# Kernel optimization log

Measured on AMD Instinct MI355X. Metric: run time of the kernel, lower is better.

The kernel has to match this reference:

```python
import jax, jax.numpy as jnp
import numpy as np

E = 262144   # number of edges
B = 8192     # buckets per grouping
D = 32       # uniform bucket degree (B*D == E)
DIM = 128    # in_feats
OUT = 128    # out_feats


def setup_inputs() -> dict:
    key = jax.random.key(0)
    ks = jax.random.split(key, 12)
    src_feat = jax.random.normal(ks[0], (E, DIM), jnp.float32)
    dst_feat = jax.random.normal(ks[1], (E, DIM), jnp.float32)
    timestamp = jax.random.uniform(ks[2], (E,), jnp.float32) * 100.0
    # grouping permutations: flat edge order -> buckets of uniform degree
    src_perm = jax.random.permutation(ks[3], E).astype(jnp.int32)
    dst_perm = jax.random.permutation(ks[4], E).astype(jnp.int32)
    # causal deg_indices: index of most recent valid temporal neighbor, <= position
    pos = jnp.arange(D, dtype=jnp.int32)[None, :]
    src_deg_indices = jnp.minimum(jax.random.randint(ks[5], (B, D), 0, D, jnp.int32), pos)
    dst_deg_indices = jnp.minimum(jax.random.randint(ks[6], (B, D), 0, D, jnp.int32), pos)
    # TimeEncodingLayer('cosine') params
    basis_freq = 0.1 * jnp.linspace(0.0, 9.0, DIM, dtype=jnp.float32)
    phase = jnp.zeros((DIM,), jnp.float32)
    W_time = jax.random.normal(ks[7], (DIM, 2 * DIM), jnp.float32) * 0.05
    b_time = jnp.zeros((DIM,), jnp.float32)
    # fc_self / fc_neigh
    W_self = jax.random.normal(ks[8], (OUT, DIM), jnp.float32) * 0.05
    b_self = jnp.zeros((OUT,), jnp.float32)
    W_neigh = jax.random.normal(ks[9], (OUT, DIM), jnp.float32) * 0.05
    b_neigh = jnp.zeros((OUT,), jnp.float32)
    return dict(src_feat=src_feat, dst_feat=dst_feat, timestamp=timestamp,
                basis_freq=basis_freq, phase=phase, W_time=W_time, b_time=b_time,
                W_self=W_self, b_self=b_self, W_neigh=W_neigh, b_neigh=b_neigh,
                src_perm=src_perm, dst_perm=dst_perm,
                src_deg_indices=src_deg_indices, dst_deg_indices=dst_deg_indices)


def _encode_time(u, t, basis_freq, phase, W_time, b_time):
    # cosine time encoding: cos(t * freq + phase), concat with u, linear, relu
    tt = jnp.cos(t[:, None] * basis_freq[None, :] + phase[None, :])  # [E, DIM]
    x = jnp.concatenate([u, tt], axis=-1) @ W_time.T + b_time
    return jax.nn.relu(x)


def _mean_conv(h_self_e, h_neigh_e, perm, idx, W_self, b_self, W_neigh, b_neigh):
    # gather flat edge features into [B, D, DIM] buckets
    hs = h_self_e[perm].reshape(B, D, DIM)
    hn = h_neigh_e[perm].reshape(B, D, DIM)
    # mean aggregator: cumsum / (deg_indices+1), then gather at deg_indices
    mean_cof = (idx.astype(hn.dtype) + 1.0)[:, :, None]          # [B, D, 1]
    h_feat = jnp.cumsum(hn, axis=1) / mean_cof                    # [B, D, DIM]
    mask_feat = jnp.take_along_axis(h_feat, idx[:, :, None], axis=1)  # [B, D, DIM]
    rst = hs @ W_self.T + b_self + mask_feat @ W_neigh.T + b_neigh    # [B, D, OUT]
    # scatter back to flat edge order
    return jnp.zeros((E, OUT), rst.dtype).at[perm].set(rst.reshape(E, OUT))


def reference(src_feat, dst_feat, timestamp, basis_freq, phase, W_time, b_time,
              W_self, b_self, W_neigh, b_neigh,
              src_perm, dst_perm, src_deg_indices, dst_deg_indices):
    enc_src = _encode_time(src_feat, timestamp, basis_freq, phase, W_time, b_time)
    enc_dst = _encode_time(dst_feat, timestamp, basis_freq, phase, W_time, b_time)
    # groupby='src': self = src embedding, neighbors = dst embeddings
    src_out = _mean_conv(enc_src, enc_dst, src_perm, src_deg_indices,
                         W_self, b_self, W_neigh, b_neigh)
    # groupby='dst': self = dst embedding, neighbors = src embeddings
    dst_out = _mean_conv(enc_dst, enc_src, dst_perm, dst_deg_indices,
                         W_self, b_self, W_neigh, b_neigh)
    return src_out, dst_out
```

## Files before the change

### kernel.cpp

```cpp
#include <hip/hip_runtime.h>
#include <hip/hip_bf16.h>
#include <math.h>

#define E_EDGES 262144
#define NBUCKET 8192
#define DEG     32
#define FDIM    128

typedef float f32x4 __attribute__((ext_vector_type(4)));
typedef short s16x8 __attribute__((ext_vector_type(8)));
typedef short s16x4 __attribute__((ext_vector_type(4)));

typedef const __attribute__((address_space(1))) unsigned g_u32;
typedef __attribute__((address_space(3))) unsigned l_u32;

__device__ __forceinline__ short f2bf(float f) {
    __hip_bfloat16 h = __float2bfloat16(f);
    return *reinterpret_cast<short*>(&h);
}
__device__ __forceinline__ float bf2f(short s) {
    union { unsigned u; float f; } v; v.u = ((unsigned)(unsigned short)s) << 16;
    return v.f;
}

__device__ __forceinline__ s16x8 read_wfrag(const short* w_lds, int n, int k0) {
    int byte = ((n << 8) + (k0 << 1)) ^ ((n & 7) << 4);
    return *reinterpret_cast<const s16x8*>(reinterpret_cast<const char*>(w_lds) + byte);
}

__device__ __forceinline__ void stage_w(short* w_lds, const float* __restrict__ Wg,
                                        int stride, int tid) {
    #pragma unroll
    for (int it = 0; it < 16; ++it) {
        int i  = it * 256 + tid;
        int n  = i >> 5;
        int k4 = (i & 31) << 2;
        const float4 v = *reinterpret_cast<const float4*>(Wg + (size_t)n * stride + k4);
        s16x4 h; h[0]=f2bf(v.x); h[1]=f2bf(v.y); h[2]=f2bf(v.z); h[3]=f2bf(v.w);
        int byte = ((n << 8) + (k4 << 1)) ^ ((n & 7) << 4);
        *reinterpret_cast<s16x4*>(reinterpret_cast<char*>(w_lds) + byte) = h;
    }
}

__device__ __forceinline__ void dma_w32k(const short* __restrict__ gsw, short* lds, int tid) {
    const int lane = tid & 63, wid = tid >> 6;
    const char* g = reinterpret_cast<const char*>(gsw);
    char* l = reinterpret_cast<char*>(lds);
    #pragma unroll
    for (int i = 0; i < 8; ++i) {
        const int off = i * 4096 + wid * 1024;
        __builtin_amdgcn_global_load_lds((g_u32*)(g + off + lane * 16),
                                         (l_u32*)(l + off), 16, 0, 0);
    }
}

__global__ void prep_kernel(const float* __restrict__ W_time,
                            const float* __restrict__ W_self,
                            const float* __restrict__ W_neigh,
                            const float* __restrict__ b_self,
                            const float* __restrict__ b_neigh,
                            short* __restrict__ Wswz,
                            float* __restrict__ bsum)
{
    const int t = blockIdx.x * 256 + threadIdx.x;
    if (t < 8192) {
        const int region = t >> 11;
        const int chunk  = t & 2047;
        const int n = chunk >> 4;
        const int c = chunk & 15;

        const float* src;
        if      (region == 0) src = W_time  + n * 256 + c * 8;
        else if (region == 1) src = W_time  + n * 256 + 128 + c * 8;
        else if (region == 2) src = W_self  + n * 128 + c * 8;
        else                  src = W_neigh + n * 128 + c * 8;

        const float4 lo = *reinterpret_cast<const float4*>(src);
        const float4 hi = *reinterpret_cast<const float4*>(src + 4);
        s16x8 h;
        h[0]=f2bf(lo.x); h[1]=f2bf(lo.y); h[2]=f2bf(lo.z); h[3]=f2bf(lo.w);
        h[4]=f2bf(hi.x); h[5]=f2bf(hi.y); h[6]=f2bf(hi.z); h[7]=f2bf(hi.w);

        const int byte = (region << 15) + ((((n << 8) + (c << 4)) ^ ((n & 7) << 4)));
        *reinterpret_cast<s16x8*>(reinterpret_cast<char*>(Wswz) + byte) = h;
    } else if (t < 8192 + 128) {
        const int c = t - 8192;
        bsum[c] = b_self[c] + b_neigh[c];
    }
}

__global__ __launch_bounds__(512, 4)
void encode_kernel(const float* __restrict__ src_feat,
                   const float* __restrict__ dst_feat,
                   const float* __restrict__ ts,
                   const float* __restrict__ freq,
                   const float* __restrict__ ph,
                   const short* __restrict__ Wswz,
                   const float* __restrict__ b_time,
                   short* __restrict__ enc_src,
                   short* __restrict__ enc_dst)
{
    __shared__ short w_lds[2][128 * 128];

    const int tid  = threadIdx.x;
    const int lane = tid & 63;
    const int wid  = tid >> 6;
    const int lrow = lane & 15;
    const int q    = lane >> 4;
    const int klo  = q << 3;
    const int r0   = blockIdx.x * 128 + wid * 16;

    float4 sf[8], df[8];
    #pragma unroll
    for (int kb = 0; kb < 4; ++kb) {
        const float* ps = src_feat + (size_t)(r0 + lrow) * FDIM + kb * 32 + klo;
        const float* pd = dst_feat + (size_t)(r0 + lrow) * FDIM + kb * 32 + klo;
        sf[kb*2]   = *reinterpret_cast<const float4*>(ps);
        sf[kb*2+1] = *reinterpret_cast<const float4*>(ps + 4);
        df[kb*2]   = *reinterpret_cast<const float4*>(pd);
        df[kb*2+1] = *reinterpret_cast<const float4*>(pd + 4);
    }

    {
        const char* g = reinterpret_cast<const char*>(Wswz);
        char* l = reinterpret_cast<char*>(&w_lds[0][0]);
        #pragma unroll
        for (int i = 0; i < 8; ++i) {
            const int off = i * 8192 + wid * 1024;
            __builtin_amdgcn_global_load_lds((g_u32*)(g + off + lane * 16),
                                             (l_u32*)(l + off), 16, 0, 0);
        }
    }

    const float t_row = ts[r0 + lrow];
    s16x8 tf[4];
    #pragma unroll
    for (int kb = 0; kb < 4; ++kb) {
        s16x8 t;
        #pragma unroll
        for (int j = 0; j < 8; ++j) {
            const int k = kb * 32 + klo + j;
            t[j] = f2bf(__cosf(fmaf(t_row, freq[k], ph[k])));
        }
        tf[kb] = t;
    }

    s16x8 as_[4], ad_[4];
    #pragma unroll
    for (int kb = 0; kb < 4; ++kb) {
        s16x8 a, b;
        #pragma unroll
        for (int j = 0; j < 4; ++j) {
            a[j]   = f2bf(sf[kb*2][j]);   a[4+j] = f2bf(sf[kb*2+1][j]);
            b[j]   = f2bf(df[kb*2][j]);   b[4+j] = f2bf(df[kb*2+1][j]);
        }
        as_[kb] = a; ad_[kb] = b;
    }
    __syncthreads();

    #pragma unroll
    for (int nt = 0; nt < 8; ++nt) {
        const int n = nt * 16 + lrow;
        f32x4 a = {0.f, 0.f, 0.f, 0.f};
        #pragma unroll
        for (int kb = 0; kb < 4; ++kb)
            a = __builtin_amdgcn_mfma_f32_16x16x32_bf16(
                    read_wfrag(w_lds[1], n, kb * 32 + klo), tf[kb], a, 0, 0, 0);
        f32x4 b = a;
        #pragma unroll
        for (int kb = 0; kb < 4; ++kb) {
            const s16x8 wf = read_wfrag(w_lds[0], n, kb * 32 + klo);
            a = __builtin_amdgcn_mfma_f32_16x16x32_bf16(wf, as_[kb], a, 0, 0, 0);
            b = __builtin_amdgcn_mfma_f32_16x16x32_bf16(wf, ad_[kb], b, 0, 0, 0);
        }
        const int ch = nt * 16 + q * 4;
        const float4 bias4 = *reinterpret_cast<const float4*>(b_time + ch);
        s16x4 ss, sd;
        #pragma unroll
        for (int r = 0; r < 4; ++r) {
            float es = a[r] + bias4[r]; es = es > 0.f ? es : 0.f;
            float ed = b[r] + bias4[r]; ed = ed > 0.f ? ed : 0.f;
            ss[r] = f2bf(es); sd[r] = f2bf(ed);
        }
        *reinterpret_cast<s16x4*>(enc_src + (size_t)(r0 + lrow) * FDIM + ch) = ss;
        *reinterpret_cast<s16x4*>(enc_dst + (size_t)(r0 + lrow) * FDIM + ch) = sd;
    }
}

__global__ __launch_bounds__(256, 2)
void encode_fallback(const float* __restrict__ src_feat,
                     const float* __restrict__ dst_feat,
                     const float* __restrict__ ts,
                     const float* __restrict__ freq,
                     const float* __restrict__ ph,
                     const float* __restrict__ W_time,
                     const float* __restrict__ b_time,
                     short* __restrict__ enc_src,
                     short* __restrict__ enc_dst)
{
    __shared__ short w_lds[128 * 128];
    const int tid  = threadIdx.x;
    const int lane = tid & 63;
    const int wid  = tid >> 6;
    const int r0   = blockIdx.x * 64 + wid * 16;
    const int lrow = lane & 15;
    const int klo  = (lane >> 4) << 3;

    stage_w(w_lds, W_time + 128, 256, tid);
    const float t_row = ts[r0 + lrow];
    s16x8 tf[4];
    #pragma unroll
    for (int kb = 0; kb < 4; ++kb) {
        const int k = kb * 32 + klo;
        s16x8 t;
        #pragma unroll
        for (int j = 0; j < 8; ++j)
            t[j] = f2bf(__cosf(fmaf(t_row, freq[k + j], ph[k + j])));
        tf[kb] = t;
    }
    __syncthreads();
    f32x4 S[8];
    #pragma unroll
    for (int nt = 0; nt < 8; ++nt) {
        f32x4 a = {0.f, 0.f, 0.f, 0.f};
        #pragma unroll
        for (int kb = 0; kb < 4; ++kb)
            a = __builtin_amdgcn_mfma_f32_16x16x32_bf16(
                    tf[kb], read_wfrag(w_lds, nt * 16 + lrow, kb * 32 + klo), a, 0, 0, 0);
        S[nt] = a;
    }
    __syncthreads();
    stage_w(w_lds, W_time, 256, tid);
    __syncthreads();
    #pragma unroll
    for (int s = 0; s < 2; ++s) {
        const float* feat = s ? dst_feat : src_feat;
        short*       enc  = s ? enc_dst  : enc_src;
        s16x8 af[4];
        #pragma unroll
        for (int kb = 0; kb < 4; ++kb) {
            const float* p = feat + (size_t)(r0 + lrow) * FDIM + kb * 32 + klo;
            const float4 lo = *reinterpret_cast<const float4*>(p);
            const float4 hi = *reinterpret_cast<const float4*>(p + 4);
            s16x8 a;
            a[0]=f2bf(lo.x); a[1]=f2bf(lo.y); a[2]=f2bf(lo.z); a[3]=f2bf(lo.w);
            a[4]=f2bf(hi.x); a[5]=f2bf(hi.y); a[6]=f2bf(hi.z); a[7]=f2bf(hi.w);
            af[kb] = a;
        }
        #pragma unroll
        for (int nt = 0; nt < 8; ++nt) {
            f32x4 acc = S[nt];
            #pragma unroll
            for (int kb = 0; kb < 4; ++kb)
                acc = __builtin_amdgcn_mfma_f32_16x16x32_bf16(
                        af[kb], read_wfrag(w_lds, nt * 16 + lrow, kb * 32 + klo), acc, 0, 0, 0);
            const int col  = nt * 16 + lrow;
            const float bias = b_time[col];
            const int rbase = r0 + ((lane >> 4) << 2);
            #pragma unroll
            for (int r = 0; r < 4; ++r) {
                float e = acc[r] + bias;
                e = e > 0.f ? e : 0.f;
                enc[(size_t)(rbase + r) * FDIM + col] = f2bf(e);
            }
        }
    }
}

template<int DMA>
__global__ __launch_bounds__(256, 3)
void conv_kernel(const short* __restrict__ enc_src,
                 const short* __restrict__ enc_dst,
                 const short* __restrict__ Wswz_self,
                 const short* __restrict__ Wswz_neigh,
                 const float* __restrict__ W_self,
                 const float* __restrict__ W_neigh,
                 const float* __restrict__ bsum,
                 const float* __restrict__ b_self,
                 const float* __restrict__ b_neigh,
                 const int* __restrict__ src_perm,
                 const int* __restrict__ dst_perm,
                 const int* __restrict__ src_idx,
                 const int* __restrict__ dst_idx,
                 float* __restrict__ out)
{
    __shared__ short w_lds[128 * 128];
    __shared__ short hf[2][DEG * 128];
    __shared__ int   perm_s[2][DEG];
    __shared__ int   idx_s[2][DEG];

    const int tid = threadIdx.x;
    const int g   = blockIdx.y;
    const int b0  = blockIdx.x * 2;

    const short* enc_self  = g ? enc_dst : enc_src;
    const short* enc_neigh = g ? enc_src : enc_dst;
    const int*   perm      = g ? dst_perm : src_perm;
    const int*   degi      = g ? dst_idx  : src_idx;
    float*       outg      = out + (size_t)g * E_EDGES * FDIM;

    if (DMA) dma_w32k(Wswz_self, w_lds, tid);

    if (tid < 64) {
        const int lb = tid >> 5, d = tid & 31;
        perm_s[lb][d] = perm[(b0 + lb) * DEG + d];
        idx_s[lb][d]  = degi[(b0 + lb) * DEG + d];
    }
    if (!DMA) stage_w(w_lds, W_self, 128, tid);
    __syncthreads();

    const int lane = tid & 63;
    const int wid  = tid >> 6;
    const int lb   = wid >> 1;
    const int mt   = wid & 1;
    const int lrow = lane & 15;
    const int q    = lane >> 4;
    const int klo  = q << 3;
    const int row  = mt * 16 + lrow;

    s16x8 hsf[4];
    {
        const int e = perm_s[lb][row];
        const short* p = enc_self + (size_t)e * FDIM;
        #pragma unroll
        for (int kb = 0; kb < 4; ++kb)
            hsf[kb] = *reinterpret_cast<const s16x8*>(p + kb * 32 + klo);
    }

    unsigned cum[DEG];
    if (wid < 2) {
        #pragma unroll
        for (int d = 0; d < DEG; ++d) {
            const int e = perm_s[wid][d];
            cum[d] = *reinterpret_cast<const unsigned*>(
                         enc_neigh + (size_t)e * FDIM + 2 * lane);
        }
    }

    f32x4 acc[8];
    #pragma unroll
    for (int nt = 0; nt < 8; ++nt) {
        f32x4 a = {0.f, 0.f, 0.f, 0.f};
        #pragma unroll
        for (int kb = 0; kb < 4; ++kb)
            a = __builtin_amdgcn_mfma_f32_16x16x32_bf16(
                    read_wfrag(w_lds, nt * 16 + lrow, kb * 32 + klo), hsf[kb], a, 0, 0, 0);
        acc[nt] = a;
    }

    if (wid < 2) {
        float run0 = 0.f, run1 = 0.f;
        #pragma unroll
        for (int d = 0; d < DEG; ++d) {
            run0 += bf2f((short)(cum[d] & 0xFFFFu));
            run1 += bf2f((short)(cum[d] >> 16));
            const float inv = __builtin_amdgcn_rcpf((float)(idx_s[wid][d] + 1));
            const unsigned pk = (unsigned)(unsigned short)f2bf(run0 * inv)
                              | ((unsigned)(unsigned short)f2bf(run1 * inv) << 16);
            const int byte = ((d << 8) + (lane << 2)) ^ ((d & 7) << 4);
            *reinterpret_cast<unsigned*>(reinterpret_cast<char*>(hf[wid]) + byte) = pk;
        }
    }

    __syncthreads();
    if (DMA) dma_w32k(Wswz_neigh, w_lds, tid);
    else     stage_w(w_lds, W_neigh, 128, tid);
    __syncthreads();

    s16x8 mff[4];
    {
        const int j = idx_s[lb][row];
        #pragma unroll
        for (int kb = 0; kb < 4; ++kb) {
            const int byte = ((j << 8) + ((kb * 32 + klo) << 1)) ^ ((j & 7) << 4);
            mff[kb] = *reinterpret_cast<const s16x8*>(
                          reinterpret_cast<const char*>(hf[lb]) + byte);
        }
    }
    #pragma unroll
    for (int nt = 0; nt < 8; ++nt) {
        f32x4 a = acc[nt];
        #pragma unroll
        for (int kb = 0; kb < 4; ++kb)
            a = __builtin_amdgcn_mfma_f32_16x16x32_bf16(
                    read_wfrag(w_lds, nt * 16 + lrow, kb * 32 + klo), mff[kb], a, 0, 0, 0);
        acc[nt] = a;
    }

    {
        const int e = perm_s[lb][row];
        float* po = outg + (size_t)e * FDIM;
        #pragma unroll
        for (int nt = 0; nt < 8; ++nt) {
            const int ch = nt * 16 + q * 4;
            float4 bs4;
            if (DMA) bs4 = *reinterpret_cast<const float4*>(bsum + ch);
            else {
                const float4 s4 = *reinterpret_cast<const float4*>(b_self + ch);
                const float4 n4 = *reinterpret_cast<const float4*>(b_neigh + ch);
                bs4 = make_float4(s4.x+n4.x, s4.y+n4.y, s4.z+n4.z, s4.w+n4.w);
            }
            f32x4 v;
            v[0] = acc[nt][0] + bs4.x; v[1] = acc[nt][1] + bs4.y;
            v[2] = acc[nt][2] + bs4.z; v[3] = acc[nt][3] + bs4.w;
            *reinterpret_cast<f32x4*>(po + ch) = v;
        }
    }
}

extern "C" void kernel_launch(void* const* d_in, const int* in_sizes, int n_in,
                              void* d_out, int out_size, void* d_ws, size_t ws_size,
                              hipStream_t stream) {
    (void)in_sizes; (void)n_in; (void)out_size;

    const float* src_feat = (const float*)d_in[0];
    const float* dst_feat = (const float*)d_in[1];
    const float* ts       = (const float*)d_in[2];
    const float* freq     = (const float*)d_in[3];
    const float* ph       = (const float*)d_in[4];
    const float* W_time   = (const float*)d_in[5];
    const float* b_time   = (const float*)d_in[6];
    const float* W_self   = (const float*)d_in[7];
    const float* b_self   = (const float*)d_in[8];
    const float* W_neigh  = (const float*)d_in[9];
    const float* b_neigh  = (const float*)d_in[10];
    const int*   src_perm = (const int*)d_in[11];
    const int*   dst_perm = (const int*)d_in[12];
    const int*   src_idx  = (const int*)d_in[13];
    const int*   dst_idx  = (const int*)d_in[14];

    short* enc_src = (short*)d_ws;
    short* enc_dst = enc_src + (size_t)E_EDGES * FDIM;
    short* Wswz    = enc_dst + (size_t)E_EDGES * FDIM;
    float* bsum    = (float*)(Wswz + 4 * 16384);
    const size_t need = (size_t)E_EDGES * FDIM * 2 * 2 + 4 * 32768 + 512;

    if (ws_size >= need) {
        prep_kernel<<<dim3(33), dim3(256), 0, stream>>>(
            W_time, W_self, W_neigh, b_self, b_neigh, Wswz, bsum);
        encode_kernel<<<dim3(E_EDGES / 128), dim3(512), 0, stream>>>(
            src_feat, dst_feat, ts, freq, ph, Wswz, b_time, enc_src, enc_dst);
        conv_kernel<1><<<dim3(NBUCKET / 2, 2), dim3(256), 0, stream>>>(
            enc_src, enc_dst, Wswz + 2 * 16384, Wswz + 3 * 16384, W_self, W_neigh,
            bsum, b_self, b_neigh, src_perm, dst_perm, src_idx, dst_idx, (float*)d_out);
    } else {
        encode_fallback<<<dim3(E_EDGES / 64), dim3(256), 0, stream>>>(
            src_feat, dst_feat, ts, freq, ph, W_time, b_time, enc_src, enc_dst);
        conv_kernel<0><<<dim3(NBUCKET / 2, 2), dim3(256), 0, stream>>>(
            enc_src, enc_dst, (const short*)nullptr, (const short*)nullptr,
            W_self, W_neigh, (const float*)nullptr, b_self, b_neigh,
            src_perm, dst_perm, src_idx, dst_idx, (float*)d_out);
    }
}
```

Measured before the change: 254.2 us.

## Project neighbor features before prefix-mean via triangular-mask MFMA

The serial per-bucket cumulative sum is removed. It used to run in two waves followed by a gather of prefix rows. Each wave now projects its own neighbor rows through W_neigh first, stores the projected rows as bf16 in LDS, and applies the causal prefix-mean as a single MFMA per output tile. That MFMA uses a lower-triangular mask vector scaled by 1/(idx[idx[row]]+1). This spreads the neighbor loads and scan work across all waves instead of serialising it in two. In exchange it adds an extra barrier and an LDS round trip of the projected values, and rounding to bf16 after projection slightly changes numerics.

Measured after the change: 257.4 us. No clear change (+1.3%).

```diff
diff --git a/kernel.cpp b/kernel.cpp
--- a/kernel.cpp
+++ b/kernel.cpp
@@ -285,7 +285,7 @@
                  float* __restrict__ out)
 {
     __shared__ short w_lds[128 * 128];
-    __shared__ short hf[2][DEG * 128];
+    __shared__ short y_lds[2][128 * 32];
     __shared__ int   perm_s[2][DEG];
     __shared__ int   idx_s[2][DEG];
 
@@ -318,22 +318,15 @@
     const int klo  = q << 3;
     const int row  = mt * 16 + lrow;
 
-    s16x8 hsf[4];
+    s16x8 hsf[4], hnf[4];
     {
         const int e = perm_s[lb][row];
-        const short* p = enc_self + (size_t)e * FDIM;
-        #pragma unroll
-        for (int kb = 0; kb < 4; ++kb)
-            hsf[kb] = *reinterpret_cast<const s16x8*>(p + kb * 32 + klo);
-    }
-
-    unsigned cum[DEG];
-    if (wid < 2) {
-        #pragma unroll
-        for (int d = 0; d < DEG; ++d) {
-            const int e = perm_s[wid][d];
-            cum[d] = *reinterpret_cast<const unsigned*>(
-                         enc_neigh + (size_t)e * FDIM + 2 * lane);
+        const short* ps = enc_self  + (size_t)e * FDIM;
+        const short* pn = enc_neigh + (size_t)e * FDIM;
+        #pragma unroll
+        for (int kb = 0; kb < 4; ++kb) {
+            hsf[kb] = *reinterpret_cast<const s16x8*>(ps + kb * 32 + klo);
+            hnf[kb] = *reinterpret_cast<const s16x8*>(pn + kb * 32 + klo);
         }
     }
 
@@ -348,43 +341,47 @@
         acc[nt] = a;
     }
 
-    if (wid < 2) {
-        float run0 = 0.f, run1 = 0.f;
-        #pragma unroll
-        for (int d = 0; d < DEG; ++d) {
-            run0 += bf2f((short)(cum[d] & 0xFFFFu));
-            run1 += bf2f((short)(cum[d] >> 16));
-            const float inv = __builtin_amdgcn_rcpf((float)(idx_s[wid][d] + 1));
-            const unsigned pk = (unsigned)(unsigned short)f2bf(run0 * inv)
-                              | ((unsigned)(unsigned short)f2bf(run1 * inv) << 16);
-            const int byte = ((d << 8) + (lane << 2)) ^ ((d & 7) << 4);
-            *reinterpret_cast<unsigned*>(reinterpret_cast<char*>(hf[wid]) + byte) = pk;
-        }
-    }
-
     __syncthreads();
     if (DMA) dma_w32k(Wswz_neigh, w_lds, tid);
     else     stage_w(w_lds, W_neigh, 128, tid);
     __syncthreads();
 
-    s16x8 mff[4];
-    {
-        const int j = idx_s[lb][row];
-        #pragma unroll
-        for (int kb = 0; kb < 4; ++kb) {
-            const int byte = ((j << 8) + ((kb * 32 + klo) << 1)) ^ ((j & 7) << 4);
-            mff[kb] = *reinterpret_cast<const s16x8*>(
-                          reinterpret_cast<const char*>(hf[lb]) + byte);
-        }
-    }
-    #pragma unroll
-    for (int nt = 0; nt < 8; ++nt) {
-        f32x4 a = acc[nt];
-        #pragma unroll
-        for (int kb = 0; kb < 4; ++kb)
-            a = __builtin_amdgcn_mfma_f32_16x16x32_bf16(
-                    read_wfrag(w_lds, nt * 16 + lrow, kb * 32 + klo), mff[kb], a, 0, 0, 0);
-        acc[nt] = a;
+    {
+        char* yb = reinterpret_cast<char*>(y_lds[lb]);
+        #pragma unroll
+        for (int nt = 0; nt < 8; ++nt) {
+            f32x4 y = {0.f, 0.f, 0.f, 0.f};
+            #pragma unroll
+            for (int kb = 0; kb < 4; ++kb)
+                y = __builtin_amdgcn_mfma_f32_16x16x32_bf16(
+                        read_wfrag(w_lds, nt * 16 + lrow, kb * 32 + klo), hnf[kb], y, 0, 0, 0);
+            const int base = (((nt * 16 + q * 4) << 6) + (row << 1)) ^ (q << 4);
+            #pragma unroll
+            for (int r = 0; r < 4; ++r)
+                *reinterpret_cast<short*>(yb + base + r * 64) = f2bf(y[r]);
+        }
+    }
+    __syncthreads();
+
+    s16x8 mf;
+    {
+        const int jd = idx_s[lb][row];
+        const int jj = idx_s[lb][jd];
+        const short invb = f2bf(__builtin_amdgcn_rcpf((float)(jj + 1)));
+        #pragma unroll
+        for (int j = 0; j < 8; ++j)
+            mf[j] = (q * 8 + j <= jd) ? invb : (short)0;
+    }
+
+    {
+        const char* yb = reinterpret_cast<const char*>(y_lds[lb]);
+        #pragma unroll
+        for (int nt = 0; nt < 8; ++nt) {
+            const int ch = nt * 16 + lrow;
+            const int abyte = ((ch << 6) + (q << 4)) ^ ((((unsigned)ch >> 2) & 3) << 4);
+            const s16x8 yf = *reinterpret_cast<const s16x8*>(yb + abyte);
+            acc[nt] = __builtin_amdgcn_mfma_f32_16x16x32_bf16(yf, mf, acc[nt], 0, 0, 0);
+        }
     }
 
     {
```
